# Optimization experiments

Hardware: AMD Instinct MI355X
Metric: run time of the kernel (lower is better)

The kernel has to match this reference:

```python
import jax, jax.numpy as jnp
import numpy as np

B, N, K = 4, 4096, 16
DP, DM = 128, 512


def _gather(points, idx):
    # points [B,N,C], idx [B,N,K] -> [B,N,K,C] (index_points)
    b, n, k = idx.shape
    flat = jnp.take_along_axis(points, idx.reshape(b, -1)[:, :, None], axis=1)
    return flat.reshape(b, n, k, points.shape[-1])


def _mlp2(x, w1, b1, w2, b2):
    return jax.nn.relu(x @ w1 + b1) @ w2 + b2


def setup_inputs():
    key = jax.random.key(0)
    ks = jax.random.split(key, 20)
    s_dp = 1.0 / np.sqrt(DP)
    s_dm = 1.0 / np.sqrt(DM)
    return {
        "xyz": jax.random.normal(ks[0], (B, N, 3), jnp.float32),
        "features": jax.random.normal(ks[1], (B, N, DP), jnp.float32),
        "fc1_w": jax.random.normal(ks[2], (DP, DM), jnp.float32) * s_dp,
        "fc1_b": jnp.zeros((DM,), jnp.float32),
        "fc2_w": jax.random.normal(ks[3], (DM, DP), jnp.float32) * s_dm,
        "fc2_b": jnp.zeros((DP,), jnp.float32),
        "wq": jax.random.normal(ks[4], (DM, DM), jnp.float32) * s_dm,
        "wk": jax.random.normal(ks[5], (DM, DM), jnp.float32) * s_dm,
        "wv": jax.random.normal(ks[6], (DM, DM), jnp.float32) * s_dm,
        "d1_w": jax.random.normal(ks[7], (3, DM), jnp.float32) * (1.0 / np.sqrt(3.0)),
        "d1_b": jnp.zeros((DM,), jnp.float32),
        "d2_w": jax.random.normal(ks[8], (DM, DM), jnp.float32) * s_dm,
        "d2_b": jnp.zeros((DM,), jnp.float32),
        "g1_w": jax.random.normal(ks[9], (DM, DM), jnp.float32) * s_dm,
        "g1_b": jnp.zeros((DM,), jnp.float32),
        "g2_w": jax.random.normal(ks[10], (DM, DM), jnp.float32) * s_dm,
        "g2_b": jnp.zeros((DM,), jnp.float32),
    }


def reference(xyz, features, fc1_w, fc1_b, fc2_w, fc2_b, wq, wk, wv,
              d1_w, d1_b, d2_w, d2_b, g1_w, g1_b, g2_w, g2_b):
    # square_distance via ||a-b||^2 = |a|^2 + |b|^2 - 2 a.b  (avoids [B,N,N,3])
    sq = jnp.sum(xyz * xyz, axis=-1)                       # [B,N]
    dists = sq[:, :, None] + sq[:, None, :] - 2.0 * jnp.einsum('bnc,bmc->bnm', xyz, xyz)
    knn_idx = jax.lax.top_k(-dists, K)[1]                  # [B,N,K] k-nearest
    knn_xyz = _gather(xyz, knn_idx)                        # [B,N,K,3]

    pre = features
    x = features @ fc1_w + fc1_b                           # [B,N,DM]
    q = x @ wq                                             # [B,N,DM]
    k = _gather(x @ wk, knn_idx)                           # [B,N,K,DM]
    v = _gather(x @ wv, knn_idx)                           # [B,N,K,DM]

    pos_enc = _mlp2(xyz[:, :, None] - knn_xyz, d1_w, d1_b, d2_w, d2_b)  # [B,N,K,DM]
    attn = _mlp2(q[:, :, None] - k + pos_enc, g1_w, g1_b, g2_w, g2_b)   # [B,N,K,DM]
    attn = jax.nn.softmax(attn / np.sqrt(DM), axis=-2)     # softmax over neighbors
    res = jnp.sum(attn * (v + pos_enc), axis=2)            # einsum bmnf,bmnf->bmf
    res = res @ fc2_w + fc2_b + pre                        # [B,N,DP]
    return res, attn
```

## Files before the change

kernel.cpp:

```cpp
#include <hip/hip_runtime.h>

#define NPTS   4096
#define NBATCH 4
#define KNN    16
#define DMODEL 512
#define DPOINT 128
#define QKVLD  1536

#define BN 128
#define BK 64

typedef unsigned short bfu;
typedef __attribute__((ext_vector_type(8))) short short8;
typedef __attribute__((ext_vector_type(4))) float f32x4;

__device__ __forceinline__ bfu f2bf(float f) {
    unsigned u = __builtin_bit_cast(unsigned, f);
    return (bfu)((u + 0x7fffu + ((u >> 16) & 1u)) >> 16);
}
__device__ __forceinline__ float bf2f(bfu h) {
    unsigned u = ((unsigned)h) << 16;
    return __builtin_bit_cast(float, u);
}

__device__ __forceinline__ void gload_lds16(const bfu* g, bfu* l) {
    __builtin_amdgcn_global_load_lds(
        (const __attribute__((address_space(1))) void*)g,
        (__attribute__((address_space(3))) void*)l, 16, 0, 0);
}

#define TPQ 8
#define QPB 32

__device__ __forceinline__ void knn_merge_level(float* bd, int* bi, int lvl)
{
    float pd[KNN]; int pi[KNN];
#pragma unroll
    for (int i = 0; i < KNN; ++i) {
        pd[i] = __shfl_xor(bd[KNN-1-i], lvl);
        pi[i] = __shfl_xor(bi[KNN-1-i], lvl);
    }
#pragma unroll
    for (int i = 0; i < KNN; ++i) {
        bool take = (pd[i] < bd[i]) || (pd[i] == bd[i] && pi[i] < bi[i]);
        if (take) { bd[i] = pd[i]; bi[i] = pi[i]; }
    }
#pragma unroll
    for (int s = 8; s >= 1; s >>= 1) {
#pragma unroll
        for (int i = 0; i < KNN; ++i) {
            if ((i & s) == 0) {
                const int j = i + s;
                bool sw = (bd[j] < bd[i]) || (bd[j] == bd[i] && bi[j] < bi[i]);
                if (sw) {
                    float td = bd[i]; bd[i] = bd[j]; bd[j] = td;
                    int   ti = bi[i]; bi[i] = bi[j]; bi[j] = ti;
                }
            }
        }
    }
}

__global__ __launch_bounds__(256) void knn_kernel(const float* __restrict__ xyz,
                                                  int* __restrict__ knn_out)
{
    __shared__ float4 pts[NPTS];
    const int b    = blockIdx.y;
    const int tid  = threadIdx.x;
    const int qloc = tid >> 3;
    const int sub  = tid & 7;
    const int n    = blockIdx.x * QPB + qloc;

    const float* bx = xyz + (size_t)b * NPTS * 3;
    for (int i = tid; i < NPTS; i += 256) {
        float x = bx[i*3+0], y = bx[i*3+1], z = bx[i*3+2];
        pts[i] = make_float4(x, y, z, x*x + y*y + z*z);
    }
    __syncthreads();

    const float4 me = pts[n];
    float bd[KNN];
    int   bi[KNN];
#pragma unroll
    for (int i = 0; i < KNN; ++i) { bd[i] = 3.4e38f; bi[i] = -1; }

    for (int t0 = 0; t0 < NPTS / TPQ; t0 += 8) {
        float d[8];
#pragma unroll
        for (int j = 0; j < 8; ++j) {
            float4 o = pts[sub + ((t0 + j) << 3)];
            d[j] = me.w + o.w - 2.f*(me.x*o.x + me.y*o.y + me.z*o.z);
        }
        float mn = fminf(fminf(fminf(d[0],d[1]),fminf(d[2],d[3])),
                         fminf(fminf(d[4],d[5]),fminf(d[6],d[7])));
        if (mn < bd[KNN-1]) {
#pragma unroll
            for (int j = 0; j < 8; ++j) {
                float dj = d[j];
                if (dj < bd[KNN-1]) {
                    const int m = sub + ((t0 + j) << 3);
#pragma unroll
                    for (int i = KNN-1; i >= 1; --i) {
                        float dp = bd[i-1];
                        if (dp > dj)        { bd[i] = dp; bi[i] = bi[i-1]; }
                        else if (bd[i] > dj){ bd[i] = dj; bi[i] = m; }
                    }
                    if (bd[0] > dj) { bd[0] = dj; bi[0] = m; }
                }
            }
        }
    }

    knn_merge_level(bd, bi, 1);
    knn_merge_level(bd, bi, 2);
    knn_merge_level(bd, bi, 4);

    int* orow = knn_out + ((size_t)b*NPTS + n) * KNN;
    const int base = b * NPTS;
    orow[sub*2+0] = base + bi[sub*2+0];
    orow[sub*2+1] = base + bi[sub*2+1];
}

__global__ __launch_bounds__(256) void cvt_bf16(const float* __restrict__ src,
                                                bfu* __restrict__ dst, int n4)
{
    int i = blockIdx.x * 256 + threadIdx.x;
    if (i < n4) {
        float4 v = ((const float4*)src)[i];
        bfu* d = dst + (size_t)i * 4;
        d[0] = f2bf(v.x); d[1] = f2bf(v.y); d[2] = f2bf(v.z); d[3] = f2bf(v.w);
    }
}

__global__ __launch_bounds__(256) void transpose_cvt(const float* __restrict__ src,
                                                     bfu* __restrict__ dst,
                                                     int K, int N)
{
    int i = blockIdx.x * 256 + threadIdx.x;
    if (i < K * N) {
        int n = i / K, k = i - n * K;
        dst[i] = f2bf(src[(size_t)k * N + n]);
    }
}

__global__ __launch_bounds__(256) void pos_h_kernel(
    const float* __restrict__ xyz, const int* __restrict__ knng,
    const float* __restrict__ d1w, const float* __restrict__ d1b,
    bfu* __restrict__ out, int row_base)
{
    const int idx  = blockIdx.x * 256 + threadIdx.x;
    const int rloc = idx >> 6;
    const int c0   = (idx & 63) * 8;
    const int grow = row_base + rloc;
    const int p    = grow >> 4;
    const int nb   = knng[grow];
    const float rx = xyz[(size_t)p*3+0] - xyz[(size_t)nb*3+0];
    const float ry = xyz[(size_t)p*3+1] - xyz[(size_t)nb*3+1];
    const float rz = xyz[(size_t)p*3+2] - xyz[(size_t)nb*3+2];
    short8 ov;
#pragma unroll
    for (int j = 0; j < 8; ++j) {
        const int k = c0 + j;
        float v = d1b[k];
        v = fmaf(rx, d1w[k],        v);
        v = fmaf(ry, d1w[512 + k],  v);
        v = fmaf(rz, d1w[1024 + k], v);
        ov[j] = (short)f2bf(fmaxf(v, 0.f));
    }
    *(short8*)&out[(size_t)rloc * DMODEL + c0] = ov;
}

__global__ __launch_bounds__(256) void attn_in_kernel(
    const int* __restrict__ knng, const bfu* __restrict__ qb,
    const bfu* __restrict__ kb, const bfu* __restrict__ posc,
    bfu* __restrict__ out, int row_base)
{
    const int idx  = blockIdx.x * 256 + threadIdx.x;
    const int rloc = idx >> 6;
    const int c0   = (idx & 63) * 8;
    const int grow = row_base + rloc;
    const int p    = grow >> 4;
    const int g    = knng[grow];
    short8 qv = *(const short8*)(qb   + (size_t)p    * QKVLD  + c0);
    short8 kv = *(const short8*)(kb   + (size_t)g    * QKVLD  + c0);
    short8 pv = *(const short8*)(posc + (size_t)rloc * DMODEL + c0);
    short8 ov;
#pragma unroll
    for (int j = 0; j < 8; ++j) {
        float v = bf2f((bfu)qv[j]) - bf2f((bfu)kv[j]) + bf2f((bfu)pv[j]);
        ov[j] = (short)f2bf(v);
    }
    *(short8*)&out[(size_t)rloc * DMODEL + c0] = ov;
}

template<int BMt, bool BIAS, bool RELU, bool OUTBF, bool RESID, bool SMAX>
__global__ __launch_bounds__(256) void gemm_mfma(
    const bfu* __restrict__ A, const bfu* __restrict__ BT,
    const float* __restrict__ bias, const float* __restrict__ resid,
    void* __restrict__ Cout, int M, int Kd, int Nd,
    const int* __restrict__ knng,
    const bfu* __restrict__ posc, const bfu* __restrict__ vb,
    bfu* __restrict__ resbuf, int row_base)
{
    constexpr int MF  = BMt / 32;
    constexpr int RPW = BMt / 4;

    __shared__ bfu As[BMt * BK];
    __shared__ bfu Bs[BN * BK];

    const int tid  = threadIdx.x;
    const int lane = tid & 63;
    const int w    = tid >> 6;

    const int nbn     = Nd / BN;
    const int q8      = gridDim.x >> 3;
    const int logical = (blockIdx.x & 7) * q8 + (blockIdx.x >> 3);
    const int bm      = (logical / nbn) * BMt;
    const int bn      = (logical % nbn) * BN;

    const int wm   = (w >> 1) * (BMt / 2);
    const int wn   = (w & 1) * 64;
    const int lrow = lane & 15;
    const int kgrp = lane >> 4;

    f32x4 acc[MF][4];
#pragma unroll
    for (int m = 0; m < MF; ++m)
#pragma unroll
        for (int n = 0; n < 4; ++n) acc[m][n] = (f32x4){0.f, 0.f, 0.f, 0.f};

    for (int k0 = 0; k0 < Kd; k0 += BK) {
        __syncthreads();

        {
            int r0 = w * 32;
            const bfu* gB = BT + (size_t)(bn + r0 + (lane >> 3)) * Kd + k0 + (lane & 7) * 8;
            bfu* lB = Bs + r0 * BK;
#pragma unroll
            for (int i = 0; i < 4; ++i)
                gload_lds16(gB + (size_t)i * 8 * Kd, lB + i * 8 * BK);
        }
        {
            int r0 = w * RPW;
            const bfu* gA = A + (size_t)(bm + r0 + (lane >> 3)) * Kd + k0 + (lane & 7) * 8;
            bfu* lA = As + r0 * BK;
#pragma unroll
            for (int i = 0; i < RPW / 8; ++i)
                gload_lds16(gA + (size_t)i * 8 * Kd, lA + i * 8 * BK);
        }

        __syncthreads();

#pragma unroll
        for (int kk = 0; kk < BK; kk += 32) {
            short8 af[MF], bfr[4];
#pragma unroll
            for (int m = 0; m < MF; ++m)
                af[m] = *(const short8*)&As[(wm + m * 16 + lrow) * BK + kk + kgrp * 8];
#pragma unroll
            for (int n = 0; n < 4; ++n)
                bfr[n] = *(const short8*)&Bs[(wn + n * 16 + lrow) * BK + kk + kgrp * 8];
#pragma unroll
            for (int m = 0; m < MF; ++m)
#pragma unroll
                for (int n = 0; n < 4; ++n)
                    acc[m][n] = __builtin_amdgcn_mfma_f32_16x16x32_bf16(
                        af[m], bfr[n], acc[m][n], 0, 0, 0);
        }
    }

    if constexpr (SMAX) {
        const float scale = 0.044194173824159216f;
#pragma unroll
        for (int m = 0; m < MF; ++m) {
            const int row0 = bm + wm + m * 16 + kgrp * 4;
            const int ploc = (bm + wm + m * 16) >> 4;
            int gnb4[4];
#pragma unroll
            for (int r = 0; r < 4; ++r) gnb4[r] = knng[(size_t)row_base + row0 + r];
#pragma unroll
            for (int n = 0; n < 4; ++n) {
                const int col = bn + wn + n * 16 + lrow;
                const float bv = bias[col];
                float v0 = (acc[m][n][0] + bv) * scale;
                float v1 = (acc[m][n][1] + bv) * scale;
                float v2 = (acc[m][n][2] + bv) * scale;
                float v3 = (acc[m][n][3] + bv) * scale;
                float mx = fmaxf(fmaxf(v0, v1), fmaxf(v2, v3));
                mx = fmaxf(mx, __shfl_xor(mx, 16));
                mx = fmaxf(mx, __shfl_xor(mx, 32));
                float e0 = __expf(v0 - mx), e1 = __expf(v1 - mx);
                float e2 = __expf(v2 - mx), e3 = __expf(v3 - mx);
                float s = e0 + e1 + e2 + e3;
                s += __shfl_xor(s, 16);
                s += __shfl_xor(s, 32);
                const float inv = 1.f / s;
                float a0 = e0*inv, a1 = e1*inv, a2 = e2*inv, a3 = e3*inv;
                float* ao = (float*)Cout;
                ao[(size_t)(row0 + 0) * DMODEL + col] = a0;
                ao[(size_t)(row0 + 1) * DMODEL + col] = a1;
                ao[(size_t)(row0 + 2) * DMODEL + col] = a2;
                ao[(size_t)(row0 + 3) * DMODEL + col] = a3;
                float res = 0.f;
                res = fmaf(a0, bf2f(vb[(size_t)gnb4[0]*QKVLD + col]) + bf2f(posc[(size_t)(row0+0)*DMODEL + col]), res);
                res = fmaf(a1, bf2f(vb[(size_t)gnb4[1]*QKVLD + col]) + bf2f(posc[(size_t)(row0+1)*DMODEL + col]), res);
                res = fmaf(a2, bf2f(vb[(size_t)gnb4[2]*QKVLD + col]) + bf2f(posc[(size_t)(row0+2)*DMODEL + col]), res);
                res = fmaf(a3, bf2f(vb[(size_t)gnb4[3]*QKVLD + col]) + bf2f(posc[(size_t)(row0+3)*DMODEL + col]), res);
                res += __shfl_xor(res, 16);
                res += __shfl_xor(res, 32);
                if (kgrp == 0) {
                    const size_t pglob = (size_t)(row_base >> 4) + ploc;
                    resbuf[pglob * DMODEL + col] = f2bf(res);
                }
            }
        }
        return;
    }

#pragma unroll
    for (int m = 0; m < MF; ++m) {
#pragma unroll
        for (int n = 0; n < 4; ++n) {
            int col = bn + wn + n * 16 + lrow;
            float bv = BIAS ? bias[col] : 0.f;
#pragma unroll
            for (int r = 0; r < 4; ++r) {
                int row = bm + wm + m * 16 + kgrp * 4 + r;
                float v = acc[m][n][r] + bv;
                if (RESID) v += resid[(size_t)row * Nd + col];
                if (RELU)  v = fmaxf(v, 0.f);
                if (OUTBF) ((bfu*)Cout)[(size_t)row * Nd + col] = f2bf(v);
                else     ((float*)Cout)[(size_t)row * Nd + col] = v;
            }
        }
    }
}

extern "C" void kernel_launch(void* const* d_in, const int* in_sizes, int n_in,
                              void* d_out, int out_size, void* d_ws, size_t ws_size,
                              hipStream_t stream)
{
    const float* xyz      = (const float*)d_in[0];
    const float* features = (const float*)d_in[1];
    const float* fc1_w    = (const float*)d_in[2];
    const float* fc1_b    = (const float*)d_in[3];
    const float* fc2_w    = (const float*)d_in[4];
    const float* fc2_b    = (const float*)d_in[5];
    const float* wq       = (const float*)d_in[6];
    const float* wk       = (const float*)d_in[7];
    const float* wv       = (const float*)d_in[8];
    const float* d1_w     = (const float*)d_in[9];
    const float* d1_b     = (const float*)d_in[10];
    const float* d2_w     = (const float*)d_in[11];
    const float* d2_b     = (const float*)d_in[12];
    const float* g1_w     = (const float*)d_in[13];
    const float* g1_b     = (const float*)d_in[14];
    const float* g2_w     = (const float*)d_in[15];
    const float* g2_b     = (const float*)d_in[16];

    const size_t Mpts  = (size_t)NBATCH * NPTS;
    const size_t Mrows = Mpts * KNN;
    float* out_res  = (float*)d_out;
    float* out_attn = (float*)d_out + Mpts * DPOINT;

    size_t off = 0;
    auto ab = [&](size_t elems) { bfu* r = (bfu*)((char*)d_ws + off); off += elems * 2; return r; };
    bfu* fc1T  = ab((size_t)DMODEL * DPOINT);
    bfu* qkvT  = ab((size_t)QKVLD * DMODEL);
    bfu* d2T   = ab((size_t)DMODEL * DMODEL);
    bfu* g1T   = ab((size_t)DMODEL * DMODEL);
    bfu* g2T   = ab((size_t)DMODEL * DMODEL);
    bfu* fc2T  = ab((size_t)DPOINT * DMODEL);
    bfu* featb = ab(Mpts * DPOINT);
    bfu* xb    = ab(Mpts * DMODEL);
    bfu* qkvb  = ab(Mpts * QKVLD);
    bfu* resb  = xb;
    int* knng  = (int*)((char*)d_ws + off); off += Mrows * 4;

    int nchunk = 32;
    {
        const int cands[4] = {4, 8, 16, 32};
        for (int i = 0; i < 4; ++i) {
            size_t need = off + 3ull * (Mrows / cands[i]) * DMODEL * 2;
            if (need <= ws_size) { nchunk = cands[i]; break; }
        }
    }
    const size_t Rc  = Mrows / nchunk;
    bfu* posc = ab(Rc * DMODEL);
    bfu* hc   = ab(Rc * DMODEL);
    bfu* ainb = ab(Rc * DMODEL);

    knn_kernel<<<dim3(NPTS/QPB, NBATCH), 256, 0, stream>>>(xyz, knng);

    transpose_cvt<<<dim3((DPOINT*DMODEL+255)/256), 256, 0, stream>>>(fc1_w, fc1T, DPOINT, DMODEL);
    transpose_cvt<<<dim3((DMODEL*DMODEL+255)/256), 256, 0, stream>>>(wq, qkvT,                 DMODEL, DMODEL);
    transpose_cvt<<<dim3((DMODEL*DMODEL+255)/256), 256, 0, stream>>>(wk, qkvT +   DMODEL*DMODEL, DMODEL, DMODEL);
    transpose_cvt<<<dim3((DMODEL*DMODEL+255)/256), 256, 0, stream>>>(wv, qkvT + 2*DMODEL*DMODEL, DMODEL, DMODEL);
    transpose_cvt<<<dim3((DMODEL*DMODEL+255)/256), 256, 0, stream>>>(d2_w, d2T, DMODEL, DMODEL);
    transpose_cvt<<<dim3((DMODEL*DMODEL+255)/256), 256, 0, stream>>>(g1_w, g1T, DMODEL, DMODEL);
    transpose_cvt<<<dim3((DMODEL*DMODEL+255)/256), 256, 0, stream>>>(g2_w, g2T, DMODEL, DMODEL);
    transpose_cvt<<<dim3((DMODEL*DPOINT+255)/256), 256, 0, stream>>>(fc2_w, fc2T, DMODEL, DPOINT);
    cvt_bf16<<<dim3((Mpts*DPOINT/4+255)/256), 256, 0, stream>>>(features, featb, (int)(Mpts*DPOINT/4));

#define GARGS(Ap, Bp, biasp, residp, Cp, M_, K_, N_, rb) \
    (Ap), (Bp), (biasp), (residp), (Cp), (int)(M_), (int)(K_), (int)(N_), \
    knng, posc, qkvb + 2*DMODEL, resb, (int)(rb)

    gemm_mfma<128, true,  false, true,  false, false><<<dim3((Mpts/128)*(DMODEL/BN)), 256, 0, stream>>>(
        GARGS(featb, fc1T, fc1_b, nullptr, xb, Mpts, DPOINT, DMODEL, 0));
    gemm_mfma<128, false, false, true,  false, false><<<dim3((Mpts/128)*(QKVLD/BN)), 256, 0, stream>>>(
        GARGS(xb, qkvT, nullptr, nullptr, qkvb, Mpts, DMODEL, QKVLD, 0));

    for (int c = 0; c < nchunk; ++c) {
        const size_t rb = (size_t)c * Rc;
        float* attn_c = out_attn + rb * DMODEL;

        pos_h_kernel<<<dim3((unsigned)(Rc/4)), 256, 0, stream>>>(xyz, knng, d1_w, d1_b, hc, (int)rb);

#define CHUNK_LAUNCH(BMT) \
        gemm_mfma<BMT, true, false, true, false, false><<<dim3((unsigned)((Rc/BMT)*(DMODEL/BN))), 256, 0, stream>>>( \
            GARGS(hc, d2T, d2_b, nullptr, posc, Rc, DMODEL, DMODEL, rb)); \
        attn_in_kernel<<<dim3((unsigned)(Rc/4)), 256, 0, stream>>>( \
            knng, qkvb, qkvb + DMODEL, posc, ainb, (int)rb); \
        gemm_mfma<BMT, true, true,  true, false, false><<<dim3((unsigned)((Rc/BMT)*(DMODEL/BN))), 256, 0, stream>>>( \
            GARGS(ainb, g1T, g1_b, nullptr, hc, Rc, DMODEL, DMODEL, rb)); \
        gemm_mfma<BMT, false, false, false, false, true><<<dim3((unsigned)((Rc/BMT)*(DMODEL/BN))), 256, 0, stream>>>( \
            GARGS(hc, g2T, g2_b, nullptr, attn_c, Rc, DMODEL, DMODEL, rb));

        if (Rc >= 32768) { CHUNK_LAUNCH(128) }
        else             { CHUNK_LAUNCH(64)  }
#undef CHUNK_LAUNCH
    }

    gemm_mfma<128, true, false, false, true, false><<<dim3((Mpts/128)*(DPOINT/BN)), 256, 0, stream>>>(
        GARGS(resb, fc2T, fc2_b, features, out_res, Mpts, DMODEL, DPOINT, 0));
#undef GARGS
}
```

Baseline: 1.988 ms.

## Fuse attention-input construction into pos-encoding GEMM epilogue and merge weight prep

Builds q - k + pos_enc inside the epilogue of the d2 GEMM, so the separate attn_in_kernel pass is gone. That pass re-read posc from global memory. The eight transpose/convert launches are also merged into one prep_weights kernel to cut launch overhead. The new epilogue does scalar bf16 gathers of q and k per element instead of the previous vectorized 8-wide loads, so those loads may coalesce less well.

```diff
diff --git a/kernel.cpp b/kernel.cpp
--- a/kernel.cpp
+++ b/kernel.cpp
@@ -121,6 +121,34 @@
     orow[sub*2+1] = base + bi[sub*2+1];
 }
 
+__global__ __launch_bounds__(256) void prep_weights(
+    const float* __restrict__ fc1_w, const float* __restrict__ wq,
+    const float* __restrict__ wk,    const float* __restrict__ wv,
+    const float* __restrict__ d2_w,  const float* __restrict__ g1_w,
+    const float* __restrict__ g2_w,  const float* __restrict__ fc2_w,
+    bfu* __restrict__ fc1T, bfu* __restrict__ qkvT, bfu* __restrict__ d2T,
+    bfu* __restrict__ g1T,  bfu* __restrict__ g2T,  bfu* __restrict__ fc2T)
+{
+    int i = blockIdx.x * 256 + threadIdx.x;
+    const int S1 = DPOINT * DMODEL;
+    const int S2 = DMODEL * DMODEL;
+    if (i < S1) { fc1T[i] = f2bf(fc1_w[(size_t)(i & 127) * DMODEL + (i >> 7)]); return; }
+    i -= S1;
+    if (i < S2) { qkvT[i]        = f2bf(wq[(size_t)(i & 511) * DMODEL + (i >> 9)]); return; }
+    i -= S2;
+    if (i < S2) { qkvT[S2 + i]   = f2bf(wk[(size_t)(i & 511) * DMODEL + (i >> 9)]); return; }
+    i -= S2;
+    if (i < S2) { qkvT[2*S2 + i] = f2bf(wv[(size_t)(i & 511) * DMODEL + (i >> 9)]); return; }
+    i -= S2;
+    if (i < S2) { d2T[i] = f2bf(d2_w[(size_t)(i & 511) * DMODEL + (i >> 9)]); return; }
+    i -= S2;
+    if (i < S2) { g1T[i] = f2bf(g1_w[(size_t)(i & 511) * DMODEL + (i >> 9)]); return; }
+    i -= S2;
+    if (i < S2) { g2T[i] = f2bf(g2_w[(size_t)(i & 511) * DMODEL + (i >> 9)]); return; }
+    i -= S2;
+    if (i < S1) { fc2T[i] = f2bf(fc2_w[(size_t)(i & 511) * DPOINT + (i >> 9)]); return; }
+}
+
 __global__ __launch_bounds__(256) void cvt_bf16(const float* __restrict__ src,
                                                 bfu* __restrict__ dst, int n4)
 {
@@ -129,17 +157,6 @@
         float4 v = ((const float4*)src)[i];
         bfu* d = dst + (size_t)i * 4;
         d[0] = f2bf(v.x); d[1] = f2bf(v.y); d[2] = f2bf(v.z); d[3] = f2bf(v.w);
-    }
-}
-
-__global__ __launch_bounds__(256) void transpose_cvt(const float* __restrict__ src,
-                                                     bfu* __restrict__ dst,
-                                                     int K, int N)
-{
-    int i = blockIdx.x * 256 + threadIdx.x;
-    if (i < K * N) {
-        int n = i / K, k = i - n * K;
-        dst[i] = f2bf(src[(size_t)k * N + n]);
     }
 }
 
@@ -170,37 +187,15 @@
     *(short8*)&out[(size_t)rloc * DMODEL + c0] = ov;
 }
 
-__global__ __launch_bounds__(256) void attn_in_kernel(
-    const int* __restrict__ knng, const bfu* __restrict__ qb,
-    const bfu* __restrict__ kb, const bfu* __restrict__ posc,
-    bfu* __restrict__ out, int row_base)
-{
-    const int idx  = blockIdx.x * 256 + threadIdx.x;
-    const int rloc = idx >> 6;
-    const int c0   = (idx & 63) * 8;
-    const int grow = row_base + rloc;
-    const int p    = grow >> 4;
-    const int g    = knng[grow];
-    short8 qv = *(const short8*)(qb   + (size_t)p    * QKVLD  + c0);
-    short8 kv = *(const short8*)(kb   + (size_t)g    * QKVLD  + c0);
-    short8 pv = *(const short8*)(posc + (size_t)rloc * DMODEL + c0);
-    short8 ov;
-#pragma unroll
-    for (int j = 0; j < 8; ++j) {
-        float v = bf2f((bfu)qv[j]) - bf2f((bfu)kv[j]) + bf2f((bfu)pv[j]);
-        ov[j] = (short)f2bf(v);
-    }
-    *(short8*)&out[(size_t)rloc * DMODEL + c0] = ov;
-}
-
-template<int BMt, bool BIAS, bool RELU, bool OUTBF, bool RESID, bool SMAX>
+template<int BMt, bool BIAS, bool RELU, bool OUTBF, bool RESID, bool AIN, bool SMAX>
 __global__ __launch_bounds__(256) void gemm_mfma(
     const bfu* __restrict__ A, const bfu* __restrict__ BT,
     const float* __restrict__ bias, const float* __restrict__ resid,
     void* __restrict__ Cout, int M, int Kd, int Nd,
     const int* __restrict__ knng,
+    const bfu* __restrict__ qb, const bfu* __restrict__ kb,
     const bfu* __restrict__ posc, const bfu* __restrict__ vb,
-    bfu* __restrict__ resbuf, int row_base)
+    bfu* __restrict__ auxb, int row_base)
 {
     constexpr int MF  = BMt / 32;
     constexpr int RPW = BMt / 4;
@@ -267,6 +262,35 @@
                     acc[m][n] = __builtin_amdgcn_mfma_f32_16x16x32_bf16(
                         af[m], bfr[n], acc[m][n], 0, 0, 0);
         }
+    }
+
+    if constexpr (AIN) {
+#pragma unroll
+        for (int m = 0; m < MF; ++m) {
+            const int row0 = bm + wm + m * 16 + kgrp * 4;
+            int p4[4], g4[4];
+#pragma unroll
+            for (int r = 0; r < 4; ++r) {
+                const int grow = row_base + row0 + r;
+                p4[r] = grow >> 4;
+                g4[r] = knng[grow];
+            }
+#pragma unroll
+            for (int n = 0; n < 4; ++n) {
+                const int col = bn + wn + n * 16 + lrow;
+                const float bv = bias[col];
+#pragma unroll
+                for (int r = 0; r < 4; ++r) {
+                    const size_t o = (size_t)(row0 + r) * DMODEL + col;
+                    bfu pb = f2bf(acc[m][n][r] + bv);
+                    ((bfu*)Cout)[o] = pb;
+                    float qv = bf2f(qb[(size_t)p4[r] * QKVLD + col]);
+                    float kv = bf2f(kb[(size_t)g4[r] * QKVLD + col]);
+                    auxb[o] = f2bf(qv - kv + bf2f(pb));
+                }
+            }
+        }
+        return;
     }
 
     if constexpr (SMAX) {
@@ -310,7 +334,7 @@
                 res += __shfl_xor(res, 32);
                 if (kgrp == 0) {
                     const size_t pglob = (size_t)(row_base >> 4) + ploc;
-                    resbuf[pglob * DMODEL + col] = f2bf(res);
+                    auxb[pglob * DMODEL + col] = f2bf(res);
                 }
             }
         }
@@ -392,24 +416,22 @@
 
     knn_kernel<<<dim3(NPTS/QPB, NBATCH), 256, 0, stream>>>(xyz, knng);
 
-    transpose_cvt<<<dim3((DPOINT*DMODEL+255)/256), 256, 0, stream>>>(fc1_w, fc1T, DPOINT, DMODEL);
-    transpose_cvt<<<dim3((DMODEL*DMODEL+255)/256), 256, 0, stream>>>(wq, qkvT,                 DMODEL, DMODEL);
-    transpose_cvt<<<dim3((DMODEL*DMODEL+255)/256), 256, 0, stream>>>(wk, qkvT +   DMODEL*DMODEL, DMODEL, DMODEL);
-    transpose_cvt<<<dim3((DMODEL*DMODEL+255)/256), 256, 0, stream>>>(wv, qkvT + 2*DMODEL*DMODEL, DMODEL, DMODEL);
-    transpose_cvt<<<dim3((DMODEL*DMODEL+255)/256), 256, 0, stream>>>(d2_w, d2T, DMODEL, DMODEL);
-    transpose_cvt<<<dim3((DMODEL*DMODEL+255)/256), 256, 0, stream>>>(g1_w, g1T, DMODEL, DMODEL);
-    transpose_cvt<<<dim3((DMODEL*DMODEL+255)/256), 256, 0, stream>>>(g2_w, g2T, DMODEL, DMODEL);
-    transpose_cvt<<<dim3((DMODEL*DPOINT+255)/256), 256, 0, stream>>>(fc2_w, fc2T, DMODEL, DPOINT);
+    {
+        const int total = 2 * DPOINT * DMODEL + 6 * DMODEL * DMODEL;
+        prep_weights<<<dim3((total + 255) / 256), 256, 0, stream>>>(
+            fc1_w, wq, wk, wv, d2_w, g1_w, g2_w, fc2_w,
+            fc1T, qkvT, d2T, g1T, g2T, fc2T);
+    }
     cvt_bf16<<<dim3((Mpts*DPOINT/4+255)/256), 256, 0, stream>>>(features, featb, (int)(Mpts*DPOINT/4));
 
-#define GARGS(Ap, Bp, biasp, residp, Cp, M_, K_, N_, rb) \
+#define GARGS(Ap, Bp, biasp, residp, Cp, M_, K_, N_, auxp, rb) \
     (Ap), (Bp), (biasp), (residp), (Cp), (int)(M_), (int)(K_), (int)(N_), \
-    knng, posc, qkvb + 2*DMODEL, resb, (int)(rb)
-
-    gemm_mfma<128, true,  false, true,  false, false><<<dim3((Mpts/128)*(DMODEL/BN)), 256, 0, stream>>>(
-        GARGS(featb, fc1T, fc1_b, nullptr, xb, Mpts, DPOINT, DMODEL, 0));
-    gemm_mfma<128, false, false, true,  false, false><<<dim3((Mpts/128)*(QKVLD/BN)), 256, 0, stream>>>(
-        GARGS(xb, qkvT, nullptr, nullptr, qkvb, Mpts, DMODEL, QKVLD, 0));
+    knng, qkvb, qkvb + DMODEL, posc, qkvb + 2*DMODEL, (auxp), (int)(rb)
+
+    gemm_mfma<128, true,  false, true,  false, false, false><<<dim3((Mpts/128)*(DMODEL/BN)), 256, 0, stream>>>(
+        GARGS(featb, fc1T, fc1_b, nullptr, xb, Mpts, DPOINT, DMODEL, resb, 0));
+    gemm_mfma<128, false, false, true,  false, false, false><<<dim3((Mpts/128)*(QKVLD/BN)), 256, 0, stream>>>(
+        GARGS(xb, qkvT, nullptr, nullptr, qkvb, Mpts, DMODEL, QKVLD, resb, 0));
 
     for (int c = 0; c < nchunk; ++c) {
         const size_t rb = (size_t)c * Rc;
@@ -418,21 +440,19 @@
         pos_h_kernel<<<dim3((unsigned)(Rc/4)), 256, 0, stream>>>(xyz, knng, d1_w, d1_b, hc, (int)rb);
 
 #define CHUNK_LAUNCH(BMT) \
-        gemm_mfma<BMT, true, false, true, false, false><<<dim3((unsigned)((Rc/BMT)*(DMODEL/BN))), 256, 0, stream>>>( \
-            GARGS(hc, d2T, d2_b, nullptr, posc, Rc, DMODEL, DMODEL, rb)); \
-        attn_in_kernel<<<dim3((unsigned)(Rc/4)), 256, 0, stream>>>( \
-            knng, qkvb, qkvb + DMODEL, posc, ainb, (int)rb); \
-        gemm_mfma<BMT, true, true,  true, false, false><<<dim3((unsigned)((Rc/BMT)*(DMODEL/BN))), 256, 0, stream>>>( \
-            GARGS(ainb, g1T, g1_b, nullptr, hc, Rc, DMODEL, DMODEL, rb)); \
-        gemm_mfma<BMT, false, false, false, false, true><<<dim3((unsigned)((Rc/BMT)*(DMODEL/BN))), 256, 0, stream>>>( \
-            GARGS(hc, g2T, g2_b, nullptr, attn_c, Rc, DMODEL, DMODEL, rb));
+        gemm_mfma<BMT, true, false, true, false, true, false><<<dim3((unsigned)((Rc/BMT)*(DMODEL/BN))), 256, 0, stream>>>( \
+            GARGS(hc, d2T, d2_b, nullptr, posc, Rc, DMODEL, DMODEL, ainb, rb)); \
+        gemm_mfma<BMT, true, true,  true, false, false, false><<<dim3((unsigned)((Rc/BMT)*(DMODEL/BN))), 256, 0, stream>>>( \
+            GARGS(ainb, g1T, g1_b, nullptr, hc, Rc, DMODEL, DMODEL, resb, rb)); \
+        gemm_mfma<BMT, false, false, false, false, false, true><<<dim3((unsigned)((Rc/BMT)*(DMODEL/BN))), 256, 0, stream>>>( \
+            GARGS(hc, g2T, g2_b, nullptr, attn_c, Rc, DMODEL, DMODEL, resb, rb));
 
         if (Rc >= 32768) { CHUNK_LAUNCH(128) }
         else             { CHUNK_LAUNCH(64)  }
 #undef CHUNK_LAUNCH
     }
 
-    gemm_mfma<128, true, false, false, true, false><<<dim3((Mpts/128)*(DPOINT/BN)), 256, 0, stream>>>(
-        GARGS(resb, fc2T, fc2_b, features, out_res, Mpts, DMODEL, DPOINT, 0));
+    gemm_mfma<128, true, false, false, true, false, false><<<dim3((Mpts/128)*(DPOINT/BN)), 256, 0, stream>>>(
+        GARGS(resb, fc2T, fc2_b, features, out_res, Mpts, DMODEL, DPOINT, resb, 0));
 #undef GARGS
 }
```

New measurement: 1.974 ms, median of 2. About the same (-0.7%).
